# Kernel optimization log

Measured on AMD Instinct MI355X. Metric: run time of the kernel, lower is better.

Reference implementation:

```python
import jax, jax.numpy as jnp
import numpy as np

C = 256        # channels per FPN level (in_channels == representation_size)
PATCH = 5      # GNN kernel_size == stride
NEG_SLOPE = 0.2
K = 7          # node_connectivities[0]


def _conv1x1(x, w, b):
    return jnp.einsum('bchw,oc->bohw', x, w) + b[None, :, None, None]


def _conv3x3(x, w, b):
    y = jax.lax.conv_general_dilated(x, w, (1, 1), 'SAME',
                                     dimension_numbers=('NCHW', 'OIHW', 'NCHW'))
    return y + b[None, :, None, None]


def _nearest(x, hout, wout):
    hin, win = x.shape[-2:]
    ih = (jnp.arange(hout) * hin) // hout
    iw = (jnp.arange(wout) * win) // wout
    return x[..., ih, :][..., iw]


def _topk_edges(score, k, n):
    # torch: A.scatter(1, topk_idx, topk_val); edge = nonzero(triu(A)); edge=[col,row]
    vals, idx = jax.lax.top_k(score, k)          # per-row top-k
    row = jnp.repeat(jnp.arange(n), k)
    col = idx.reshape(-1)
    val = vals.reshape(-1)
    # triu keeps col>=row; GATv2Conv removes self loops then re-adds one per node
    mask = (col > row) & (val != 0.0)
    loop = jnp.arange(n)
    src = jnp.concatenate([col, loop])           # PyG edge_index[0] = source
    dst = jnp.concatenate([row, loop])
    emask = jnp.concatenate([mask, jnp.ones((n,), bool)])
    return src, dst, emask


def _gatv2(x, src, dst, emask, wl, bl, wr, br, att, bias, n):
    heads, dout = att.shape
    xl = (x @ wl + bl).reshape(n, heads, dout)   # source transform (lin_l)
    xr = (x @ wr + br).reshape(n, heads, dout)   # target transform (lin_r)
    m = xl[src] + xr[dst]                        # [E, H, D]
    e = jnp.sum(jax.nn.leaky_relu(m, NEG_SLOPE) * att[None], axis=-1)  # [E, H]
    e = jnp.where(emask[:, None], e, -1e30)
    emax = jax.ops.segment_max(e, dst, num_segments=n)
    w = jnp.exp(e - emax[dst]) * emask[:, None]
    denom = jax.ops.segment_sum(w, dst, num_segments=n)
    alpha = w / (denom[dst] + 1e-16)
    out = jax.ops.segment_sum(alpha[..., None] * xl[src], dst, num_segments=n)
    return out.reshape(n, heads * dout) + bias


def _gnn(x, p, k):
    # x: [1, C, H, W], H,W divisible by PATCH
    _, c, hh, ww = x.shape
    nh, nw = hh // PATCH, ww // PATCH
    n = nh * nw
    patches = x[0].reshape(c, nh, PATCH, nw, PATCH).transpose(1, 3, 0, 2, 4)
    patches = patches.reshape(n, c, PATCH, PATCH)
    emb = jax.nn.relu(jnp.einsum('ncij,ocij->no', patches, p['conv1_w']) + p['conv1_b'])
    emb = jax.nn.relu(emb @ p['fc2_w'].T + p['fc2_b'])
    # feature-similarity kNN graph
    src, dst, em = _topk_edges(emb @ emb.T, k, n)
    h = jax.nn.elu(_gatv2(emb, src, dst, em, *p['g1'], n))
    h = jax.nn.elu(_gatv2(h, src, dst, em, *p['g2'], n))
    # spatial kNN graph (k smallest distances; self distance 0 drops out via val!=0)
    ii, jj = jnp.meshgrid(jnp.arange(nh) * PATCH, jnp.arange(nw) * PATCH, indexing='ij')
    centers = jnp.stack([ii.reshape(-1), jj.reshape(-1)], -1).astype(x.dtype)
    dist = jnp.sqrt(jnp.sum((centers[:, None] - centers[None]) ** 2, -1))
    src2, dst2, em2 = _topk_edges(-dist, k, n)
    h2 = jax.nn.elu(_gatv2(emb, src2, dst2, em2, *p['g3'], n))
    h2 = jax.nn.elu(_gatv2(h2, src2, dst2, em2, *p['g4'], n))
    hc = jax.nn.relu(jnp.concatenate([h, h2], 1) @ p['fc3_w'].T + p['fc3_b']) + h2
    # torch: reshape(dim,dim,C).swapdims(-1,0) -> [C, nw, nh]
    grid = jnp.transpose(hc.reshape(nh, nw, c), (2, 1, 0))
    # ConvTranspose2d(C, C, 5, stride=5): non-overlapping tiling
    up = jnp.einsum('cij,coab->oiajb', grid, p['convT_w'])
    up = up.reshape(c, nw * PATCH, nh * PATCH) + p['convT_b'][:, None, None]
    return jax.nn.relu(up)[None]


def _forward(feat0, feat1, inner_w, inner_b, layer_w, layer_b, convT_w, convT_b,
             conv1_w, conv1_b, fc2_w, fc2_b, fc3_w, fc3_b,
             g1_wl, g1_bl, g1_wr, g1_br, g1_att, g1_bias,
             g2_wl, g2_bl, g2_wr, g2_br, g2_att, g2_bias,
             g3_wl, g3_bl, g3_wr, g3_br, g3_att, g3_bias,
             g4_wl, g4_bl, g4_wr, g4_br, g4_att, g4_bias, k):
    feats = [feat0, feat1]
    xs = []
    for i, f in enumerate(feats):
        p = dict(conv1_w=conv1_w[i], conv1_b=conv1_b[i],
                 fc2_w=fc2_w[i], fc2_b=fc2_b[i],
                 fc3_w=fc3_w[i], fc3_b=fc3_b[i],
                 convT_w=convT_w[i], convT_b=convT_b[i],
                 g1=(g1_wl[i], g1_bl[i], g1_wr[i], g1_br[i], g1_att[i], g1_bias[i]),
                 g2=(g2_wl[i], g2_bl[i], g2_wr[i], g2_br[i], g2_att[i], g2_bias[i]),
                 g3=(g3_wl[i], g3_bl[i], g3_wr[i], g3_br[i], g3_att[i], g3_bias[i]),
                 g4=(g4_wl[i], g4_bl[i], g4_wr[i], g4_br[i], g4_att[i], g4_bias[i]))
        xs.append(f + _gnn(f, p, k))
    # top-down FPN
    last = _conv1x1(xs[1], inner_w[1], inner_b[1])
    out1 = _conv3x3(last, layer_w[1], layer_b[1])
    inner0 = _conv1x1(xs[0], inner_w[0], inner_b[0])
    td = _nearest(last, xs[0].shape[-2], xs[0].shape[-1])
    out0 = _conv3x3(inner0 + td, layer_w[0], layer_b[0])
    return out0, out1


def setup_inputs() -> dict:
    key = jax.random.key(0)
    keys = jax.random.split(key, 48)
    it = iter(range(48))
    def rn(shape, s=0.05):
        return (jax.random.normal(keys[next(it)], shape) * s).astype(jnp.float32)
    H8 = 8 * C
    inp = dict(
        feat0=rn((1, C, 200, 200), 1.0),
        feat1=rn((1, C, 100, 100), 1.0),
        inner_w=rn((2, C, C)), inner_b=rn((2, C)),
        layer_w=rn((2, C, C, 3, 3)), layer_b=rn((2, C)),
        convT_w=rn((2, C, C, PATCH, PATCH)), convT_b=rn((2, C)),
        conv1_w=rn((2, C, C, PATCH, PATCH)), conv1_b=rn((2, C)),
        fc2_w=rn((2, C, C)), fc2_b=rn((2, C)),
        fc3_w=rn((2, C, 2 * C)), fc3_b=rn((2, C)),
        g1_wl=rn((2, C, H8)), g1_bl=rn((2, H8)), g1_wr=rn((2, C, H8)), g1_br=rn((2, H8)),
        g1_att=rn((2, 8, C)), g1_bias=rn((2, H8)),
        g2_wl=rn((2, H8, C)), g2_bl=rn((2, C)), g2_wr=rn((2, H8, C)), g2_br=rn((2, C)),
        g2_att=rn((2, 1, C)), g2_bias=rn((2, C)),
        g3_wl=rn((2, C, H8)), g3_bl=rn((2, H8)), g3_wr=rn((2, C, H8)), g3_br=rn((2, H8)),
        g3_att=rn((2, 8, C)), g3_bias=rn((2, H8)),
        g4_wl=rn((2, H8, C)), g4_bl=rn((2, C)), g4_wr=rn((2, H8, C)), g4_br=rn((2, C)),
        g4_att=rn((2, 1, C)), g4_bias=rn((2, C)),
        k=K,
    )
    return inp


def reference(feat0, feat1, inner_w, inner_b, layer_w, layer_b, convT_w, convT_b,
              conv1_w, conv1_b, fc2_w, fc2_b, fc3_w, fc3_b,
              g1_wl, g1_bl, g1_wr, g1_br, g1_att, g1_bias,
              g2_wl, g2_bl, g2_wr, g2_br, g2_att, g2_bias,
              g3_wl, g3_bl, g3_wr, g3_br, g3_att, g3_bias,
              g4_wl, g4_bl, g4_wr, g4_br, g4_att, g4_bias, k):
    return _forward(feat0, feat1, inner_w, inner_b, layer_w, layer_b, convT_w, convT_b,
                    conv1_w, conv1_b, fc2_w, fc2_b, fc3_w, fc3_b,
                    g1_wl, g1_bl, g1_wr, g1_br, g1_att, g1_bias,
                    g2_wl, g2_bl, g2_wr, g2_br, g2_att, g2_bias,
                    g3_wl, g3_bl, g3_wr, g3_br, g3_att, g3_bias,
                    g4_wl, g4_bl, g4_wr, g4_br, g4_att, g4_bias, k)
```

## Files before the change

kernel.cpp:

```cpp
#include <hip/hip_runtime.h>
#include <cstdint>
#include <cstddef>
#include <math.h>

#define KNN 7

using short8  = __attribute__((ext_vector_type(8))) short;
using floatx4 = __attribute__((ext_vector_type(4))) float;

static const size_t OFF_ARENA = 0;
static const size_t OFF_XS0   = 10240000;
static const size_t OFF_XS1   = 20480000;
static const size_t OFF_LAST  = 23040000;
static const size_t OFF_EMB   = 25600000;
static const size_t OFF_EMB2  = 26009600;
static const size_t OFF_XL    = 26419200;
static const size_t OFF_H1    = 32972800;
static const size_t OFF_XL2   = 36249600;
static const size_t OFF_CAT   = 37068800;
static const size_t OFF_HC    = 37888000;
static const size_t OFF_SRCF  = 38400000;
static const size_t OFF_SRCS  = 38411200;
static const size_t OFF_BF_A  = 38422400;
static const size_t OFF_BF_W  = 40122400;

static __device__ __forceinline__ unsigned short f2bf(float f) {
    union { float f; unsigned u; } v; v.f = f;
    unsigned u = v.u;
    unsigned r = u + 0x7fffu + ((u >> 16) & 1u);
    return (unsigned short)(r >> 16);
}

static __device__ __forceinline__ void glds16(const void* g, void* l) {
    __builtin_amdgcn_global_load_lds((const __attribute__((address_space(1))) void*)g,
                                     (__attribute__((address_space(3))) void*)l, 16, 0, 0);
}

template<int ACT, bool BIAS>
__global__ __launch_bounds__(256)
void gemm_k(const float* __restrict__ A, const float* __restrict__ B,
            const float* __restrict__ bias, float* __restrict__ C, int M, int N, int K)
{
    __shared__ float As[16][68];
    __shared__ float Bs[16][68];
    const int tid = threadIdx.x;
    const int bm0 = blockIdx.y * 64;
    const int bn0 = blockIdx.x * 64;
    const int tx = tid & 15, ty = tid >> 4;
    const int lrow = tid >> 2;
    const int lk4  = (tid & 3) << 2;
    const int m = bm0 + lrow;
    const int nn = bn0 + lrow;
    const bool aok = m < M, bok = nn < N;
    float acc[4][4] = {{0.f,0.f,0.f,0.f},{0.f,0.f,0.f,0.f},{0.f,0.f,0.f,0.f},{0.f,0.f,0.f,0.f}};

    float4 va = {0.f,0.f,0.f,0.f}, vb = {0.f,0.f,0.f,0.f};
    if (aok) va = *(const float4*)(A + (size_t)m * K + lk4);
    if (bok) vb = *(const float4*)(B + (size_t)nn * K + lk4);

    for (int k0 = 0; k0 < K; k0 += 16) {
        As[lk4+0][lrow]=va.x; As[lk4+1][lrow]=va.y; As[lk4+2][lrow]=va.z; As[lk4+3][lrow]=va.w;
        Bs[lk4+0][lrow]=vb.x; Bs[lk4+1][lrow]=vb.y; Bs[lk4+2][lrow]=vb.z; Bs[lk4+3][lrow]=vb.w;
        __syncthreads();
        float4 na = {0.f,0.f,0.f,0.f}, nb = {0.f,0.f,0.f,0.f};
        const bool more = (k0 + 16) < K;
        if (more) {
            if (aok) na = *(const float4*)(A + (size_t)m * K + (k0 + 16 + lk4));
            if (bok) nb = *(const float4*)(B + (size_t)nn * K + (k0 + 16 + lk4));
        }
        #pragma unroll
        for (int k = 0; k < 16; k++) {
            const float4 av = *(const float4*)&As[k][ty << 2];
            const float4 bv = *(const float4*)&Bs[k][tx << 2];
            const float a0=av.x,a1=av.y,a2=av.z,a3=av.w;
            const float b0=bv.x,b1=bv.y,b2=bv.z,b3=bv.w;
            acc[0][0]=fmaf(a0,b0,acc[0][0]); acc[0][1]=fmaf(a0,b1,acc[0][1]);
            acc[0][2]=fmaf(a0,b2,acc[0][2]); acc[0][3]=fmaf(a0,b3,acc[0][3]);
            acc[1][0]=fmaf(a1,b0,acc[1][0]); acc[1][1]=fmaf(a1,b1,acc[1][1]);
            acc[1][2]=fmaf(a1,b2,acc[1][2]); acc[1][3]=fmaf(a1,b3,acc[1][3]);
            acc[2][0]=fmaf(a2,b0,acc[2][0]); acc[2][1]=fmaf(a2,b1,acc[2][1]);
            acc[2][2]=fmaf(a2,b2,acc[2][2]); acc[2][3]=fmaf(a2,b3,acc[2][3]);
            acc[3][0]=fmaf(a3,b0,acc[3][0]); acc[3][1]=fmaf(a3,b1,acc[3][1]);
            acc[3][2]=fmaf(a3,b2,acc[3][2]); acc[3][3]=fmaf(a3,b3,acc[3][3]);
        }
        __syncthreads();
        va = na; vb = nb;
    }
    #pragma unroll
    for (int i = 0; i < 4; i++) {
        const int mm = bm0 + (ty << 2) + i;
        if (mm >= M) continue;
        #pragma unroll
        for (int jj = 0; jj < 4; jj++) {
            const int nc = bn0 + (tx << 2) + jj;
            if (nc >= N) continue;
            float v = acc[i][jj];
            if (BIAS) v += bias[nc];
            if (ACT == 1) v = fmaxf(v, 0.f);
            C[(size_t)mm * N + nc] = v;
        }
    }
}

template<int ACT, bool BIAS>
static inline void gemm32(hipStream_t s, const float* A, const float* B, const float* bias,
                          float* C, int M, int N, int K)
{
    dim3 g((N + 63) / 64, (M + 63) / 64);
    gemm_k<ACT, BIAS><<<g, dim3(256), 0, s>>>(A, B, bias, C, M, N, K);
}

__global__ __launch_bounds__(256)
void gemm32_sk_k(const float* __restrict__ A, const float* __restrict__ B,
                 float* __restrict__ part, int M, int N, int K, int Kc)
{
    __shared__ float As[16][68];
    __shared__ float Bs[16][68];
    const int tid = threadIdx.x;
    const int bm0 = blockIdx.y * 64;
    const int bn0 = blockIdx.x * 64;
    const int sblk = blockIdx.z;
    const int kbeg = sblk * Kc;
    const int kend = (kbeg + Kc < K) ? kbeg + Kc : K;
    const int tx = tid & 15, ty = tid >> 4;
    const int lrow = tid >> 2;
    const int lk4  = (tid & 3) << 2;
    const int m = bm0 + lrow;
    const int nn = bn0 + lrow;
    const bool aok = m < M, bok = nn < N;
    float acc[4][4] = {{0.f,0.f,0.f,0.f},{0.f,0.f,0.f,0.f},{0.f,0.f,0.f,0.f},{0.f,0.f,0.f,0.f}};

    float4 va = {0.f,0.f,0.f,0.f}, vb = {0.f,0.f,0.f,0.f};
    if (aok) va = *(const float4*)(A + (size_t)m * K + kbeg + lk4);
    if (bok) vb = *(const float4*)(B + (size_t)nn * K + kbeg + lk4);

    for (int k0 = kbeg; k0 < kend; k0 += 16) {
        As[lk4+0][lrow]=va.x; As[lk4+1][lrow]=va.y; As[lk4+2][lrow]=va.z; As[lk4+3][lrow]=va.w;
        Bs[lk4+0][lrow]=vb.x; Bs[lk4+1][lrow]=vb.y; Bs[lk4+2][lrow]=vb.z; Bs[lk4+3][lrow]=vb.w;
        __syncthreads();
        float4 na = {0.f,0.f,0.f,0.f}, nb = {0.f,0.f,0.f,0.f};
        const bool more = (k0 + 16) < kend;
        if (more) {
            if (aok) na = *(const float4*)(A + (size_t)m * K + (k0 + 16 + lk4));
            if (bok) nb = *(const float4*)(B + (size_t)nn * K + (k0 + 16 + lk4));
        }
        #pragma unroll
        for (int k = 0; k < 16; k++) {
            const float4 av = *(const float4*)&As[k][ty << 2];
            const float4 bv = *(const float4*)&Bs[k][tx << 2];
            const float a0=av.x,a1=av.y,a2=av.z,a3=av.w;
            const float b0=bv.x,b1=bv.y,b2=bv.z,b3=bv.w;
            acc[0][0]=fmaf(a0,b0,acc[0][0]); acc[0][1]=fmaf(a0,b1,acc[0][1]);
            acc[0][2]=fmaf(a0,b2,acc[0][2]); acc[0][3]=fmaf(a0,b3,acc[0][3]);
            acc[1][0]=fmaf(a1,b0,acc[1][0]); acc[1][1]=fmaf(a1,b1,acc[1][1]);
            acc[1][2]=fmaf(a1,b2,acc[1][2]); acc[1][3]=fmaf(a1,b3,acc[1][3]);
            acc[2][0]=fmaf(a2,b0,acc[2][0]); acc[2][1]=fmaf(a2,b1,acc[2][1]);
            acc[2][2]=fmaf(a2,b2,acc[2][2]); acc[2][3]=fmaf(a2,b3,acc[2][3]);
            acc[3][0]=fmaf(a3,b0,acc[3][0]); acc[3][1]=fmaf(a3,b1,acc[3][1]);
            acc[3][2]=fmaf(a3,b2,acc[3][2]); acc[3][3]=fmaf(a3,b3,acc[3][3]);
        }
        __syncthreads();
        va = na; vb = nb;
    }
    float* P = part + (size_t)sblk * M * N;
    #pragma unroll
    for (int i = 0; i < 4; i++) {
        const int mm = bm0 + (ty << 2) + i;
        if (mm >= M) continue;
        #pragma unroll
        for (int jj = 0; jj < 4; jj++) {
            const int nc = bn0 + (tx << 2) + jj;
            if (nc >= N) continue;
            P[(size_t)mm * N + nc] = acc[i][jj];
        }
    }
}

template<int ACT, bool BIAS>
__global__ void sk_reduce_k(const float* __restrict__ part, const float* __restrict__ bias,
                            float* __restrict__ C, int MN, int N, int S)
{
    const int i4 = (blockIdx.x * 256 + threadIdx.x) * 4;
    if (i4 >= MN) return;
    float4 a = *(const float4*)(part + i4);
    for (int s = 1; s < S; s++) {
        const float4 b = *(const float4*)(part + (size_t)s * MN + i4);
        a.x += b.x; a.y += b.y; a.z += b.z; a.w += b.w;
    }
    if (BIAS) {
        const int n = i4 % N;
        a.x += bias[n]; a.y += bias[n + 1]; a.z += bias[n + 2]; a.w += bias[n + 3];
    }
    if (ACT == 1) {
        a.x = fmaxf(a.x, 0.f); a.y = fmaxf(a.y, 0.f);
        a.z = fmaxf(a.z, 0.f); a.w = fmaxf(a.w, 0.f);
    }
    *(float4*)(C + i4) = a;
}

template<int ACT, bool BIAS>
static inline void gemm32_sk(hipStream_t s, const float* A, const float* B, const float* bias,
                             float* C, float* part, int M, int N, int K, int S)
{
    const int Kc = ((K / S + 15) / 16) * 16;
    dim3 g((N + 63) / 64, (M + 63) / 64, S);
    gemm32_sk_k<<<g, dim3(256), 0, s>>>(A, B, part, M, N, K, Kc);
    const int MN = M * N;
    sk_reduce_k<ACT, BIAS><<<dim3((MN / 4 + 255) / 256), dim3(256), 0, s>>>(part, bias, C, MN, N, S);
}

enum { BT_NT = 0, BT_CONV2 = 2 };


template<int BT, int ACT, int BAX, bool ADDMAT>
__global__ __launch_bounds__(256)
void bgemm_k(const unsigned short* __restrict__ A, const unsigned short* __restrict__ B,
             const float* __restrict__ bias, const float* __restrict__ bias2, int nsplit,
             const float* __restrict__ Dmat, int Dld,
             float* __restrict__ C, int M, int N, int K, int imH, int imW)
{
    __shared__ unsigned short As[2][4096];
    __shared__ unsigned short Bs[2][4096];
    const int tid  = threadIdx.x;
    const int lane = tid & 63;
    const int wid  = tid >> 6;
    const int quad = lane >> 4;
    const int l15  = lane & 15;
    const int wy = wid >> 1, wx = wid & 1;
    const int bm0 = blockIdx.y * 128;
    const int bn0 = blockIdx.x * 128;

    floatx4 zero = {0.f, 0.f, 0.f, 0.f};
    floatx4 acc[4][4];
    #pragma unroll
    for (int i = 0; i < 4; i++)
        #pragma unroll
        for (int j = 0; j < 4; j++) acc[i][j] = zero;

    const int l4 = lane >> 2, sc = lane & 3;
    const int r0 = wid * 32 + l4;
    const int r1 = r0 + 16;
    int am0 = bm0 + r0; if (am0 > M - 1) am0 = M - 1;
    int am1 = bm0 + r1; if (am1 > M - 1) am1 = M - 1;
    const unsigned short* aP0 = A + (size_t)am0 * K + sc * 8;
    const unsigned short* aP1 = A + (size_t)am1 * K + sc * 8;

    const unsigned short* bP0 = A;
    const unsigned short* bP1 = A;
    if (BT == BT_NT) {
        int bn0r = bn0 + r0; if (bn0r > N - 1) bn0r = N - 1;
        int bn1r = bn0 + r1; if (bn1r > N - 1) bn1r = N - 1;
        bP0 = B + (size_t)bn0r * K + sc * 8;
        bP1 = B + (size_t)bn1r * K + sc * 8;
    }

    const int crow  = tid >> 1;
    const int chalf = (tid & 1) << 4;
    int cy = 0, cx = 0;
    if (BT == BT_CONV2) {
        int pp = bn0 + crow; if (pp > N - 1) pp = N - 1;
        cy = pp / imW; cx = pp - cy * imW;
    }

    auto stageA = [&](int buf, int k0) {
        glds16(aP0 + k0, &As[buf][(wid * 2 + 0) * 512]);
        glds16(aP1 + k0, &As[buf][(wid * 2 + 1) * 512]);
    };
    auto stageB = [&](int buf, int k0) {
        glds16(bP0 + k0, &Bs[buf][(wid * 2 + 0) * 512]);
        glds16(bP1 + k0, &Bs[buf][(wid * 2 + 1) * 512]);
    };
    auto ldB_conv = [&](int k0, uint4& q0, uint4& q1) {
        const int jj = k0 >> 8;
        const int j3 = jj / 3;
        const int dy = j3 - 1, dx = jj - j3 * 3 - 1;
        const int c0 = k0 & 255;
        const int yy = cy + dy, xx = cx + dx;
        q0 = (uint4){0, 0, 0, 0}; q1 = (uint4){0, 0, 0, 0};
        if ((unsigned)yy < (unsigned)imH && (unsigned)xx < (unsigned)imW) {
            const uint4* p = (const uint4*)(B + (((size_t)yy * imW + xx) << 8) + c0 + chalf);
            q0 = p[0]; q1 = p[1];
        }
    };
    auto wrB = [&](int buf, const uint4& q0, const uint4& q1) {
        *(uint4*)&Bs[buf][crow * 32 + chalf]     = q0;
        *(uint4*)&Bs[buf][crow * 32 + chalf + 8] = q1;
    };
    auto compute = [&](int buf) {
        short8 af[4], bfr[4];
        #pragma unroll
        for (int i = 0; i < 4; i++)
            af[i] = *(const short8*)&As[buf][(wy * 64 + i * 16 + l15) * 32 + quad * 8];
        #pragma unroll
        for (int j = 0; j < 4; j++)
            bfr[j] = *(const short8*)&Bs[buf][(wx * 64 + j * 16 + l15) * 32 + quad * 8];
        #pragma unroll
        for (int i = 0; i < 4; i++)
            #pragma unroll
            for (int j = 0; j < 4; j++)
                acc[i][j] = __builtin_amdgcn_mfma_f32_16x16x32_bf16(af[i], bfr[j], acc[i][j], 0, 0, 0);
    };

    if (BT == BT_NT) {
        stageA(0, 0); stageB(0, 0);
        int bufc = 0;
        for (int k0 = 0; k0 < K; k0 += 32) {
            __syncthreads();
            if (k0 + 32 < K) { stageA(bufc ^ 1, k0 + 32); stageB(bufc ^ 1, k0 + 32); }
            compute(bufc);
            bufc ^= 1;
        }
    } else {
        uint4 b00, b01, b10, b11;
        ldB_conv(0, b00, b01);
        if (32 < K) ldB_conv(32, b10, b11);
        stageA(0, 0); wrB(0, b00, b01);
        for (int k0 = 0; k0 < K; k0 += 64) {
            __syncthreads();
            if (k0 + 64 < K) ldB_conv(k0 + 64, b00, b01);
            if (k0 + 32 < K) { stageA(1, k0 + 32); wrB(1, b10, b11); }
            compute(0);
            if (k0 + 32 < K) {
                __syncthreads();
                if (k0 + 96 < K) ldB_conv(k0 + 96, b10, b11);
                if (k0 + 64 < K) { stageA(0, k0 + 64); wrB(0, b00, b01); }
                compute(1);
            }
        }
    }

    #pragma unroll
    for (int i = 0; i < 4; i++) {
        #pragma unroll
        for (int r = 0; r < 4; r++) {
            const int m = bm0 + wy * 64 + i * 16 + quad * 4 + r;
            if (m >= M) continue;
            #pragma unroll
            for (int j = 0; j < 4; j++) {
                const int n = bn0 + wx * 64 + j * 16 + l15;
                if (n >= N) continue;
                float v = acc[i][j][r];
                if (bias != nullptr)
                    v += (BAX == 0) ? bias[m] : (n < nsplit ? bias[n] : bias2[n - nsplit]);
                if (ACT == 1) v = fmaxf(v, 0.f);
                if (ADDMAT) v += Dmat[(size_t)m * Dld + n];
                C[(size_t)m * N + n] = v;
            }
        }
    }
}

template<int BT, int ACT, int BAX, bool ADDMAT>
static inline void bgemm(hipStream_t s, const unsigned short* A, const unsigned short* B,
                         const float* bias, const float* bias2, int nsplit,
                         const float* D, int Dld, float* C,
                         int M, int N, int K, int imH = 0, int imW = 0)
{
    dim3 g((N + 127) / 128, (M + 127) / 128);
    bgemm_k<BT, ACT, BAX, ADDMAT><<<g, dim3(256), 0, s>>>(A, B, bias, bias2, nsplit,
                                                          D, Dld, C, M, N, K, imH, imW);
}

__global__ __launch_bounds__(256)
void bgemm_sk_k(const unsigned short* __restrict__ A, const unsigned short* __restrict__ B,
                float* __restrict__ part, int M, int N, int K, int Kc)
{
    __shared__ unsigned short As[2][4096];
    __shared__ unsigned short Bs[2][4096];
    const int tid  = threadIdx.x;
    const int lane = tid & 63;
    const int wid  = tid >> 6;
    const int quad = lane >> 4;
    const int l15  = lane & 15;
    const int wy = wid >> 1, wx = wid & 1;
    const int bm0 = blockIdx.y * 128;
    const int bn0 = blockIdx.x * 128;
    const int kbeg = blockIdx.z * Kc;
    const int kend = (kbeg + Kc < K) ? kbeg + Kc : K;

    floatx4 zero = {0.f, 0.f, 0.f, 0.f};
    floatx4 acc[4][4];
    #pragma unroll
    for (int i = 0; i < 4; i++)
        #pragma unroll
        for (int j = 0; j < 4; j++) acc[i][j] = zero;

    const int l4 = lane >> 2, sc = lane & 3;
    const int r0 = wid * 32 + l4;
    const int r1 = r0 + 16;
    int am0 = bm0 + r0; if (am0 > M - 1) am0 = M - 1;
    int am1 = bm0 + r1; if (am1 > M - 1) am1 = M - 1;
    int bn0r = bn0 + r0; if (bn0r > N - 1) bn0r = N - 1;
    int bn1r = bn0 + r1; if (bn1r > N - 1) bn1r = N - 1;
    const unsigned short* aP0 = A + (size_t)am0 * K + sc * 8;
    const unsigned short* aP1 = A + (size_t)am1 * K + sc * 8;
    const unsigned short* bP0 = B + (size_t)bn0r * K + sc * 8;
    const unsigned short* bP1 = B + (size_t)bn1r * K + sc * 8;

    auto stageA = [&](int buf, int k0) {
        glds16(aP0 + k0, &As[buf][(wid * 2 + 0) * 512]);
        glds16(aP1 + k0, &As[buf][(wid * 2 + 1) * 512]);
    };
    auto stageB = [&](int buf, int k0) {
        glds16(bP0 + k0, &Bs[buf][(wid * 2 + 0) * 512]);
        glds16(bP1 + k0, &Bs[buf][(wid * 2 + 1) * 512]);
    };
    auto compute = [&](int buf) {
        short8 af[4], bfr[4];
        #pragma unroll
        for (int i = 0; i < 4; i++)
            af[i] = *(const short8*)&As[buf][(wy * 64 + i * 16 + l15) * 32 + quad * 8];
        #pragma unroll
        for (int j = 0; j < 4; j++)
            bfr[j] = *(const short8*)&Bs[buf][(wx * 64 + j * 16 + l15) * 32 + quad * 8];
        #pragma unroll
        for (int i = 0; i < 4; i++)
            #pragma unroll
            for (int j = 0; j < 4; j++)
                acc[i][j] = __builtin_amdgcn_mfma_f32_16x16x32_bf16(af[i], bfr[j], acc[i][j], 0, 0, 0);
    };

    stageA(0, kbeg); stageB(0, kbeg);
    int bufc = 0;
    for (int k0 = kbeg; k0 < kend; k0 += 32) {
        __syncthreads();
        if (k0 + 32 < kend) { stageA(bufc ^ 1, k0 + 32); stageB(bufc ^ 1, k0 + 32); }
        compute(bufc);
        bufc ^= 1;
    }

    float* P = part + (size_t)blockIdx.z * M * N;
    #pragma unroll
    for (int i = 0; i < 4; i++) {
        #pragma unroll
        for (int r = 0; r < 4; r++) {
            const int m = bm0 + wy * 64 + i * 16 + quad * 4 + r;
            if (m >= M) continue;
            #pragma unroll
            for (int j = 0; j < 4; j++) {
                const int n = bn0 + wx * 64 + j * 16 + l15;
                if (n >= N) continue;
                P[(size_t)m * N + n] = acc[i][j][r];
            }
        }
    }
}

template<int ACT, bool ADDMAT>
__global__ void bsk_reduce_k(const float* __restrict__ part,
                             const float* __restrict__ bias, const float* __restrict__ bias2,
                             int nsplit, const float* __restrict__ Dmat, int Dld,
                             float* __restrict__ C, int MN, int N, int S)
{
    const int i4 = (blockIdx.x * 256 + threadIdx.x) * 4;
    if (i4 >= MN) return;
    float4 a = *(const float4*)(part + i4);
    for (int s = 1; s < S; s++) {
        const float4 b = *(const float4*)(part + (size_t)s * MN + i4);
        a.x += b.x; a.y += b.y; a.z += b.z; a.w += b.w;
    }
    const int n = i4 % N;
    const float* bb = (n < nsplit) ? (bias + n) : (bias2 + n - nsplit);
    a.x += bb[0]; a.y += bb[1]; a.z += bb[2]; a.w += bb[3];
    if (ACT == 1) {
        a.x = fmaxf(a.x, 0.f); a.y = fmaxf(a.y, 0.f);
        a.z = fmaxf(a.z, 0.f); a.w = fmaxf(a.w, 0.f);
    }
    if (ADDMAT) {
        const int m = i4 / N;
        const float4 d = *(const float4*)(Dmat + (size_t)m * Dld + n);
        a.x += d.x; a.y += d.y; a.z += d.z; a.w += d.w;
    }
    *(float4*)(C + i4) = a;
}

template<int ACT, bool ADDMAT>
static inline void bgemm_sk(hipStream_t s, const unsigned short* A, const unsigned short* B,
                            const float* bias, const float* bias2, int nsplit,
                            const float* D, int Dld, float* C, float* part,
                            int M, int N, int K, int S)
{
    const int Kc = ((K / S + 31) / 32) * 32;
    dim3 g((N + 127) / 128, (M + 127) / 128, S);
    bgemm_sk_k<<<g, dim3(256), 0, s>>>(A, B, part, M, N, K, Kc);
    const int MN = M * N;
    bsk_reduce_k<ACT, ADDMAT><<<dim3((MN / 4 + 255) / 256), dim3(256), 0, s>>>(
        part, bias, bias2, nsplit, D, Dld, C, MN, N, S);
}

__global__ void cast_bf16_k(const float* __restrict__ in, unsigned short* __restrict__ out, int total)
{
    const int i4 = (blockIdx.x * 256 + threadIdx.x) * 4;
    if (i4 + 4 <= total) {
        const float4 v = *(const float4*)(in + i4);
        ushort4 o;
        o.x = f2bf(v.x); o.y = f2bf(v.y); o.z = f2bf(v.z); o.w = f2bf(v.w);
        *(ushort4*)(out + i4) = o;
    } else {
        for (int i = i4; i < total; i++) out[i] = f2bf(in[i]);
    }
}

static inline void cast_bf(hipStream_t s, const float* in, unsigned short* out, int total)
{
    cast_bf16_k<<<dim3((total / 4 + 255) / 256), dim3(256), 0, s>>>(in, out, total);
}

__device__ __forceinline__ void cast_t_body(const float* __restrict__ in,
                                            unsigned short* __restrict__ out, int K, int N)
{
    __shared__ float tile[64][65];
    const int n0 = blockIdx.x * 64;
    const int k0 = blockIdx.y * 64;
    const int t = threadIdx.x;
    const int r = t >> 2;
    const int c4 = (t & 3) << 4;
    {
        const int k = k0 + r;
        if (k < K && n0 + c4 + 16 <= N) {
            const float4* p = (const float4*)(in + (size_t)k * N + n0 + c4);
            *(float4*)&tile[r][c4]      = p[0];
            *(float4*)&tile[r][c4 + 4]  = p[1];
            *(float4*)&tile[r][c4 + 8]  = p[2];
            *(float4*)&tile[r][c4 + 12] = p[3];
        } else {
            for (int i = 0; i < 16; i++)
                tile[r][c4 + i] = (k < K && n0 + c4 + i < N) ? in[(size_t)k * N + n0 + c4 + i] : 0.f;
        }
    }
    __syncthreads();
    const int n = n0 + r;
    if (n >= N) return;
    unsigned short tmp[16];
    #pragma unroll
    for (int i = 0; i < 16; i++) tmp[i] = f2bf(tile[c4 + i][r]);
    if (k0 + 64 <= K) {
        *(uint4*)(out + (size_t)n * K + k0 + c4)     = *(uint4*)&tmp[0];
        *(uint4*)(out + (size_t)n * K + k0 + c4 + 8) = *(uint4*)&tmp[8];
    } else {
        for (int i = 0; i < 16; i++)
            if (k0 + c4 + i < K) out[(size_t)n * K + k0 + c4 + i] = tmp[i];
    }
}

__global__ void cast_t_k(const float* __restrict__ in, unsigned short* __restrict__ out, int K, int N)
{
    cast_t_body(in, out, K, N);
}

__global__ void cast_t2_k(const float* __restrict__ in0, const float* __restrict__ in1,
                          unsigned short* __restrict__ out0, unsigned short* __restrict__ out1,
                          int K, int N)
{
    if (blockIdx.z == 0) cast_t_body(in0, out0, K, N);
    else                 cast_t_body(in1, out1, K, N);
}

static inline void cast_t(hipStream_t s, const float* in, unsigned short* out, int K, int N)
{
    cast_t_k<<<dim3((N + 63) / 64, (K + 63) / 64), dim3(256), 0, s>>>(in, out, K, N);
}

static inline void cast_t2(hipStream_t s, const float* in0, const float* in1,
                           unsigned short* out0, unsigned short* out1, int K, int N)
{
    cast_t2_k<<<dim3((N + 63) / 64, (K + 63) / 64, 2), dim3(256), 0, s>>>(in0, in1, out0, out1, K, N);
}

__global__ void reorder_w3_k(const float* __restrict__ in, unsigned short* __restrict__ out)
{
    const int idx = blockIdx.x * 256 + threadIdx.x;
    if (idx >= 589824) return;
    const int o = idx / 2304;
    const int r = idx - o * 2304;
    const int j = r >> 8;
    const int c = r & 255;
    out[idx] = f2bf(in[(size_t)o * 2304 + c * 9 + j]);
}

__global__ void extract_patches_k(const float* __restrict__ f, float* __restrict__ patches,
                                  int nw, int H, int total)
{
    int idx = blockIdx.x * 256 + threadIdx.x;
    if (idx >= total) return;
    int q = idx % 6400;
    int p = idx / 6400;
    int c = q / 25;
    int rem = q - c * 25;
    int a = rem / 5, b = rem - (rem / 5) * 5;
    int ih = p / nw, iw = p - (p / nw) * nw;
    patches[idx] = f[(size_t)c * H * H + (size_t)(ih * 5 + a) * H + (iw * 5 + b)];
}

__global__ void topk_feat_k(const float* __restrict__ score, int* __restrict__ srcCols, int n)
{
    const int r = blockIdx.x;
    const int lane = threadIdx.x;
    const float* row = score + (size_t)r * n;
    int   sel[KNN];
    float selv[KNN];
    #pragma unroll
    for (int t = 0; t < KNN; t++) {
        float best = -__builtin_huge_valf();
        int   bidx = 0x7fffffff;
        for (int c = lane; c < n; c += 64) {
            bool taken = false;
            #pragma unroll
            for (int u = 0; u < KNN; u++)
                if (u < t && sel[u] == c) taken = true;
            if (taken) continue;
            float v = row[c];
            if (v > best || (v == best && c < bidx)) { best = v; bidx = c; }
        }
        #pragma unroll
        for (int off = 32; off > 0; off >>= 1) {
            float ov = __shfl_down(best, off);
            int   oi = __shfl_down(bidx, off);
            if (ov > best || (ov == best && oi < bidx)) { best = ov; bidx = oi; }
        }
        best = __shfl(best, 0);
        bidx = __shfl(bidx, 0);
        sel[t] = bidx; selv[t] = best;
    }
    if (lane < KNN) {
        int c = -1; float v = 0.f;
        #pragma unroll
        for (int t = 0; t < KNN; t++)
            if (lane == t) { c = sel[t]; v = selv[t]; }
        srcCols[r * KNN + lane] = (c > r && v != 0.0f) ? c : -1;
    }
}

__global__ void topk_spatial_k(int* __restrict__ srcCols, int n, int nw)
{
    const int r = blockIdx.x;
    const int lane = threadIdx.x;
    const int ri = r / nw, rj = r - (r / nw) * nw;
    int sel[KNN];
    #pragma unroll
    for (int t = 0; t < KNN; t++) {
        int bkey = 0x7fffffff;
        for (int c = lane; c < n; c += 64) {
            bool taken = false;
            #pragma unroll
            for (int u = 0; u < KNN; u++)
                if (u < t && sel[u] == c) taken = true;
            if (taken) continue;
            const int ci = c / nw, cj = c - (c / nw) * nw;
            const int dy = (ri - ci) * 5, dx = (rj - cj) * 5;
            const int d2 = dy * dy + dx * dx;
            const int key = (d2 << 11) | c;
            if (key < bkey) bkey = key;
        }
        #pragma unroll
        for (int off = 32; off > 0; off >>= 1) {
            int ok = __shfl_down(bkey, off);
            if (ok < bkey) bkey = ok;
        }
        bkey = __shfl(bkey, 0);
        sel[t] = bkey & 2047;
    }
    if (lane < KNN) {
        int c = -1;
        #pragma unroll
        for (int t = 0; t < KNN; t++) if (lane == t) c = sel[t];
        srcCols[r * KNN + lane] = (c > r) ? c : -1;
    }
}

__global__ void gat_fused_k(const float* __restrict__ x, int xroff, int xstride,
                            const float* __restrict__ att,
                            const int* __restrict__ srcCols, const float* __restrict__ bias,
                            float* __restrict__ out, int n, int H, int ostride, int ooff)
{
    const int wid = (blockIdx.x * blockDim.x + threadIdx.x) >> 6;
    const int lane = threadIdx.x & 63;
    if (wid >= n * H) return;
    const int h = wid % H;
    const int r = wid / H;
    const int d0 = lane << 2;

    const float4 xrf  = *(const float4*)(x + (size_t)r * xstride + xroff + h * 256 + d0);
    const float4 attf = *(const float4*)(att + (size_t)h * 256 + d0);

    int srcs[8];
    #pragma unroll
    for (int s_ = 0; s_ < KNN; s_++) srcs[s_] = srcCols[r * KNN + s_];
    srcs[7] = r;

    float4 xlf[8];
    float  e[8];
    #pragma unroll
    for (int s_ = 0; s_ < 8; s_++) {
        const int c = srcs[s_];
        float4 v = {0.f, 0.f, 0.f, 0.f};
        if (c >= 0) v = *(const float4*)(x + (size_t)c * xstride + h * 256 + d0);
        xlf[s_] = v;
        float m, p = 0.f;
        m = v.x + xrf.x; m = (m > 0.f) ? m : 0.2f * m; p += m * attf.x;
        m = v.y + xrf.y; m = (m > 0.f) ? m : 0.2f * m; p += m * attf.y;
        m = v.z + xrf.z; m = (m > 0.f) ? m : 0.2f * m; p += m * attf.z;
        m = v.w + xrf.w; m = (m > 0.f) ? m : 0.2f * m; p += m * attf.w;
        #pragma unroll
        for (int off = 32; off > 0; off >>= 1) p += __shfl_down(p, off);
        e[s_] = __shfl(p, 0);
    }

    float mx = e[7];
    #pragma unroll
    for (int s_ = 0; s_ < KNN; s_++)
        if (srcs[s_] >= 0) mx = fmaxf(mx, e[s_]);
    float a[8], denom = 0.f;
    #pragma unroll
    for (int s_ = 0; s_ < 8; s_++) {
        a[s_] = (s_ == 7 || srcs[s_] >= 0) ? expf(e[s_] - mx) : 0.f;
        denom += a[s_];
    }
    const float inv = 1.f / (denom + 1e-16f);

    float o0 = 0.f, o1 = 0.f, o2 = 0.f, o3 = 0.f;
    #pragma unroll
    for (int s_ = 0; s_ < 8; s_++) {
        const float al = a[s_] * inv;
        o0 = fmaf(al, xlf[s_].x, o0); o1 = fmaf(al, xlf[s_].y, o1);
        o2 = fmaf(al, xlf[s_].z, o2); o3 = fmaf(al, xlf[s_].w, o3);
    }
    const float* bb = bias + (size_t)h * 256 + d0;
    o0 += bb[0]; o1 += bb[1]; o2 += bb[2]; o3 += bb[3];
    o0 = (o0 > 0.f) ? o0 : (expf(o0) - 1.f);
    o1 = (o1 > 0.f) ? o1 : (expf(o1) - 1.f);
    o2 = (o2 > 0.f) ? o2 : (expf(o2) - 1.f);
    o3 = (o3 > 0.f) ? o3 : (expf(o3) - 1.f);
    float4 res = {o0, o1, o2, o3};
    *(float4*)(out + (size_t)r * ostride + ooff + (size_t)h * 256 + d0) = res;
}

__global__ void scatter_convT_k(const float* __restrict__ f, const float* __restrict__ U,
                                const float* __restrict__ bias, float* __restrict__ xs,
                                int nw, int H, int total)
{
    int idx = blockIdx.x * 256 + threadIdx.x;
    if (idx >= total) return;
    int x = idx % H;
    int t = idx / H;
    int y = t % H;
    int o = t / H;
    int j = y / 5, a = y - j * 5;
    int i = x / 5, b = x - i * 5;
    int p = i * nw + j;
    float v = U[(size_t)p * 6400 + o * 25 + a * 5 + b] + bias[o];
    v = fmaxf(v, 0.f);
    xs[idx] = f[idx] + v;
}

__global__ void upsample_add_k(float* __restrict__ acc, const float* __restrict__ last,
                               int H, int Hs, int total)
{
    int idx = blockIdx.x * 256 + threadIdx.x;
    if (idx >= total) return;
    int x = idx % H;
    int t = idx / H;
    int y = t % H;
    int c = t / H;
    acc[idx] += last[(size_t)c * Hs * Hs + (size_t)(y >> 1) * Hs + (x >> 1)];
}

static void run_level(void* const* d_in, float* ws, int l, int H, hipStream_t s)
{
    const float* f = (const float*)d_in[l];
    const int nh = H / 5, nw = nh, n = nh * nw, HW = H * H;

    const float* convT_w = (const float*)d_in[6]  + (size_t)l * 1638400;
    const float* convT_b = (const float*)d_in[7]  + l * 256;
    const float* conv1_w = (const float*)d_in[8]  + (size_t)l * 1638400;
    const float* conv1_b = (const float*)d_in[9]  + l * 256;
    const float* fc2_w   = (const float*)d_in[10] + (size_t)l * 65536;
    const float* fc2_b   = (const float*)d_in[11] + l * 256;
    const float* fc3_w   = (const float*)d_in[12] + (size_t)l * 131072;
    const float* fc3_b   = (const float*)d_in[13] + l * 256;
    const float* g1_wl   = (const float*)d_in[14] + (size_t)l * 524288;
    const float* g1_bl   = (const float*)d_in[15] + l * 2048;
    const float* g1_wr   = (const float*)d_in[16] + (size_t)l * 524288;
    const float* g1_br   = (const float*)d_in[17] + l * 2048;
    const float* g1_att  = (const float*)d_in[18] + l * 2048;
    const float* g1_bias = (const float*)d_in[19] + l * 2048;
    const float* g2_wl   = (const float*)d_in[20] + (size_t)l * 524288;
    const float* g2_bl   = (const float*)d_in[21] + l * 256;
    const float* g2_wr   = (const float*)d_in[22] + (size_t)l * 524288;
    const float* g2_br   = (const float*)d_in[23] + l * 256;
    const float* g2_att  = (const float*)d_in[24] + l * 256;
    const float* g2_bias = (const float*)d_in[25] + l * 256;
    const float* g3_wl   = (const float*)d_in[26] + (size_t)l * 524288;
    const float* g3_bl   = (const float*)d_in[27] + l * 2048;
    const float* g3_wr   = (const float*)d_in[28] + (size_t)l * 524288;
    const float* g3_br   = (const float*)d_in[29] + l * 2048;
    const float* g3_att  = (const float*)d_in[30] + l * 2048;
    const float* g3_bias = (const float*)d_in[31] + l * 2048;
    const float* g4_wl   = (const float*)d_in[32] + (size_t)l * 524288;
    const float* g4_bl   = (const float*)d_in[33] + l * 256;
    const float* g4_wr   = (const float*)d_in[34] + (size_t)l * 524288;
    const float* g4_br   = (const float*)d_in[35] + l * 256;
    const float* g4_att  = (const float*)d_in[36] + l * 256;
    const float* g4_bias = (const float*)d_in[37] + l * 256;

    float* patches = ws + OFF_ARENA;
    float* xs    = ws + (l == 0 ? OFF_XS0 : OFF_XS1);
    float* emb   = ws + OFF_EMB;
    float* emb2  = ws + OFF_EMB2;
    float* score = ws + OFF_LAST;
    float* xlr   = ws + OFF_XL;
    float* h1    = ws + OFF_H1;
    float* xlr2  = ws + OFF_XL2;
    float* cat   = ws + OFF_CAT;
    float* hc    = ws + OFF_HC;
    int* srcF = (int*)(ws + OFF_SRCF);
    int* srcS = (int*)(ws + OFF_SRCS);
    unsigned short* ba = (unsigned short*)(ws + OFF_BF_A);
    unsigned short* bw = (unsigned short*)(ws + OFF_BF_W);
    float* part = ws + OFF_ARENA;

    { int tot = n * 6400;
      extract_patches_k<<<dim3((tot + 255) / 256), dim3(256), 0, s>>>(f, patches, nw, H, tot); }

    gemm32_sk<1, true>(s, patches, conv1_w, conv1_b, emb, xlr, n, 256, 6400, 16);
    gemm32<1, true>(s, emb, fc2_w, fc2_b, emb2, n, 256, 256);
    gemm32<0, false>(s, emb2, emb2, nullptr, score, n, n, 256);
    topk_feat_k<<<dim3(n), dim3(64), 0, s>>>(score, srcF, n);
    topk_spatial_k<<<dim3(n), dim3(64), 0, s>>>(srcS, n, nw);

    const int gatw1 = n * 8;
    const int gatw2 = n;

    cast_bf(s, emb2, ba, n * 256);
    cast_t2(s, g1_wl, g1_wr, bw, bw + 2048 * 256, 256, 2048);
    if (n >= 1024)
        bgemm<BT_NT, 0, 1, false>(s, ba, bw, g1_bl, g1_br, 2048, nullptr, 0, xlr, n, 4096, 256);
    else
        bgemm_sk<0, false>(s, ba, bw, g1_bl, g1_br, 2048, nullptr, 0, xlr, part, n, 4096, 256, 2);
    gat_fused_k<<<dim3((gatw1 + 3) / 4), dim3(256), 0, s>>>(xlr, 2048, 4096, g1_att, srcF, g1_bias, h1, n, 8, 2048, 0);

    cast_bf(s, h1, ba, n * 2048);
    cast_t2(s, g2_wl, g2_wr, bw, bw + 256 * 2048, 2048, 256);
    bgemm_sk<0, false>(s, ba, bw, g2_bl, g2_br, 256, nullptr, 0, xlr2, part, n, 512, 2048, 8);
    gat_fused_k<<<dim3((gatw2 + 3) / 4), dim3(256), 0, s>>>(xlr2, 256, 512, g2_att, srcF, g2_bias, cat, n, 1, 512, 0);

    cast_bf(s, emb2, ba, n * 256);
    cast_t2(s, g3_wl, g3_wr, bw, bw + 2048 * 256, 256, 2048);
    if (n >= 1024)
        bgemm<BT_NT, 0, 1, false>(s, ba, bw, g3_bl, g3_br, 2048, nullptr, 0, xlr, n, 4096, 256);
    else
        bgemm_sk<0, false>(s, ba, bw, g3_bl, g3_br, 2048, nullptr, 0, xlr, part, n, 4096, 256, 2);
    gat_fused_k<<<dim3((gatw1 + 3) / 4), dim3(256), 0, s>>>(xlr, 2048, 4096, g3_att, srcS, g3_bias, h1, n, 8, 2048, 0);

    cast_bf(s, h1, ba, n * 2048);
    cast_t2(s, g4_wl, g4_wr, bw, bw + 256 * 2048, 2048, 256);
    bgemm_sk<0, false>(s, ba, bw, g4_bl, g4_br, 256, nullptr, 0, xlr2, part, n, 512, 2048, 8);
    gat_fused_k<<<dim3((gatw2 + 3) / 4), dim3(256), 0, s>>>(xlr2, 256, 512, g4_att, srcS, g4_bias, cat, n, 1, 512, 256);

    cast_bf(s, cat, ba, n * 512);
    cast_bf(s, fc3_w, bw, 131072);
    bgemm_sk<1, true>(s, ba, bw, fc3_b, fc3_b, 256, cat + 256, 512, hc, part, n, 256, 512, 4);
    cast_bf(s, hc, ba, n * 256);
    cast_t(s, convT_w, bw, 256, 6400);
    bgemm<BT_NT, 0, 1, false>(s, ba, bw, nullptr, nullptr, 0, nullptr, 0, patches, n, 6400, 256);
    { int tot = 256 * HW;
      scatter_convT_k<<<dim3((tot + 255) / 256), dim3(256), 0, s>>>(f, patches, convT_b, xs, nw, H, tot); }
}

extern "C" void kernel_launch(void* const* d_in, const int* in_sizes, int n_in,
                              void* d_out, int out_size, void* d_ws, size_t ws_size,
                              hipStream_t stream)
{
    float* ws  = (float*)d_ws;
    float* out = (float*)d_out;

    run_level(d_in, ws, 0, 200, stream);
    run_level(d_in, ws, 1, 100, stream);

    const float* inner_w = (const float*)d_in[2];
    const float* inner_b = (const float*)d_in[3];
    const float* layer_w = (const float*)d_in[4];
    const float* layer_b = (const float*)d_in[5];
    float* xs0    = ws + OFF_XS0;
    float* xs1    = ws + OFF_XS1;
    float* last   = ws + OFF_LAST;
    float* inner0 = ws + OFF_ARENA;
    unsigned short* bimg = (unsigned short*)(ws + OFF_XL);
    unsigned short* bw1  = (unsigned short*)(ws + OFF_BF_W);
    unsigned short* bwc  = (unsigned short*)(ws + OFF_BF_W + 100000);

    cast_t(stream, xs1, bimg, 256, 10000);
    cast_bf(stream, inner_w + 65536, bw1, 65536);
    bgemm<BT_NT, 0, 0, false>(stream, bw1, bimg, inner_b + 256, nullptr, 0, nullptr, 0,
                              last, 256, 10000, 256);
    reorder_w3_k<<<dim3((589824 + 255) / 256), dim3(256), 0, stream>>>(layer_w + 589824, bwc);
    cast_t(stream, last, bimg, 256, 10000);
    bgemm<BT_CONV2, 0, 0, false>(stream, bwc, bimg, layer_b + 256, nullptr, 0, nullptr, 0,
                                 out + 10240000, 256, 10000, 2304, 100, 100);

    cast_t(stream, xs0, bimg, 256, 40000);
    cast_bf(stream, inner_w, bw1, 65536);
    bgemm<BT_NT, 0, 0, false>(stream, bw1, bimg, inner_b, nullptr, 0, nullptr, 0,
                              inner0, 256, 40000, 256);
    { int tot = 256 * 40000;
      upsample_add_k<<<dim3((tot + 255) / 256), dim3(256), 0, stream>>>(inner0, last, 200, 100, tot); }
    reorder_w3_k<<<dim3((589824 + 255) / 256), dim3(256), 0, stream>>>(layer_w, bwc);
    cast_t(stream, inner0, bimg, 256, 40000);
    bgemm<BT_CONV2, 0, 0, false>(stream, bwc, bimg, layer_b, nullptr, 0, nullptr, 0,
                                 out, 256, 40000, 2304, 200, 200);
}
```

Before: 1.231 ms.

## Deepen conv GEMM B prefetch to three stages and remap blocks across XCDs

```diff
diff --git a/kernel.cpp b/kernel.cpp
--- a/kernel.cpp
+++ b/kernel.cpp
@@ -227,8 +227,19 @@
     const int quad = lane >> 4;
     const int l15  = lane & 15;
     const int wy = wid >> 1, wx = wid & 1;
-    const int bm0 = blockIdx.y * 128;
-    const int bn0 = blockIdx.x * 128;
+
+    int bxx = blockIdx.x, byy = blockIdx.y;
+    if (BT == BT_CONV2) {
+        const int nbx = gridDim.x;
+        const int nwg = nbx * 2;
+        const int hw  = byy * nbx + bxx;
+        const int q = nwg >> 3, r = nwg & 7;
+        const int x8 = hw & 7, d = hw >> 3;
+        const int lg = (x8 < r) ? x8 * (q + 1) + d : r * (q + 1) + (x8 - r) * q + d;
+        byy = lg & 1; bxx = lg >> 1;
+    }
+    const int bm0 = byy * 128;
+    const int bn0 = bxx * 128;
 
     floatx4 zero = {0.f, 0.f, 0.f, 0.f};
     floatx4 acc[4][4];
@@ -311,21 +322,26 @@
             bufc ^= 1;
         }
     } else {
-        uint4 b00, b01, b10, b11;
-        ldB_conv(0, b00, b01);
-        if (32 < K) ldB_conv(32, b10, b11);
-        stageA(0, 0); wrB(0, b00, b01);
-        for (int k0 = 0; k0 < K; k0 += 64) {
+        const int T = K >> 5;
+        uint4 r0a, r0b, r1a, r1b, r2a, r2b;
+        ldB_conv(0,  r0a, r0b);
+        ldB_conv(32, r1a, r1b);
+        ldB_conv(64, r2a, r2b);
+        stageA(0, 0);
+        wrB(0, r0a, r0b);
+        auto body = [&](int t, uint4& ca, uint4& cb, uint4& la, uint4& lb) {
             __syncthreads();
-            if (k0 + 64 < K) ldB_conv(k0 + 64, b00, b01);
-            if (k0 + 32 < K) { stageA(1, k0 + 32); wrB(1, b10, b11); }
-            compute(0);
-            if (k0 + 32 < K) {
-                __syncthreads();
-                if (k0 + 96 < K) ldB_conv(k0 + 96, b10, b11);
-                if (k0 + 64 < K) { stageA(0, k0 + 64); wrB(0, b00, b01); }
-                compute(1);
+            if (t + 3 < T) ldB_conv((t + 3) << 5, la, lb);
+            if (t + 1 < T) {
+                stageA((t + 1) & 1, (t + 1) << 5);
+                wrB((t + 1) & 1, ca, cb);
             }
+            compute(t & 1);
+        };
+        for (int t = 0; t < T; t += 3) {
+            body(t,     r1a, r1b, r0a, r0b);
+            body(t + 1, r2a, r2b, r1a, r1b);
+            body(t + 2, r0a, r0b, r2a, r2b);
         }
     }
 
```

After: 1.209 ms. No clear change (-1.8%).
